# Optimization experiments

Hardware: AMD Instinct MI355X
Metric: run time of the kernel (lower is better)

Reference implementation:

```python
import jax, jax.numpy as jnp
import numpy as np

B, N, Q, H = 32, 1024, 64, 768


def setup_inputs() -> dict:
    key = jax.random.key(0)
    k1, k2, k3, k4 = jax.random.split(key, 4)
    return {
        "nodes_compress": jax.random.normal(k1, (B, N, H), dtype=jnp.float32),
        "query_compress": jax.random.normal(k2, (B, Q, H), dtype=jnp.float32),
        "nodes_hidden": jax.random.normal(k3, (B, N, H), dtype=jnp.float32),
        # nn.Linear(3H, 1, bias=False).weight flattened to (3H,)
        "w": jax.random.normal(k4, (3 * H,), dtype=jnp.float32) * (1.0 / np.sqrt(3 * H)),
    }


def reference(nodes_compress, query_compress, nodes_hidden, w):
    h = nodes_compress.shape[-1]
    w_n, w_q, w_nq = w[:h], w[h:2 * h], w[2 * h:]
    # Decomposed trilinear similarity: identical to Linear([n, q, n*q]) -> scalar
    sim = (
        (nodes_compress @ w_n)[:, :, None]          # (B, N, 1)
        + (query_compress @ w_q)[:, None, :]        # (B, 1, Q)
        + jnp.einsum("bnh,bqh,h->bnq", nodes_compress, query_compress, w_nq)
    )                                                # (B, N, Q)
    # nodes -> query attention
    a = jax.nn.softmax(sim, axis=-1)                 # (B, N, Q)
    nodes2query = jnp.einsum("bnq,bqh->bnh", a, query_compress)
    # query -> nodes attention (max over query, softmax over nodes)
    b = jax.nn.softmax(jnp.max(sim, axis=-1), axis=-1)  # (B, N)
    q2n = jnp.einsum("bn,bnh->bh", b, nodes_compress)[:, None, :]  # (B, 1, H)
    q2n = jnp.broadcast_to(q2n, nodes_compress.shape)               # (B, N, H)
    return jnp.concatenate(
        [nodes_compress, nodes2query, nodes_compress * nodes2query, nodes_compress * q2n],
        axis=-1,
    )  # (B, N, 4H)
```

## Files before the change

### kernel.cpp

```cpp
#include <hip/hip_runtime.h>
#include <hip/hip_bf16.h>

#define BB 32
#define NN 1024
#define QQ 64
#define HH 768

typedef __attribute__((ext_vector_type(8))) short short8;
typedef __attribute__((ext_vector_type(4))) float f32x4;

__device__ __forceinline__ unsigned short f2b(float f) {
  unsigned int u = __float_as_uint(f);
  unsigned int r = u + 0x7fffu + ((u >> 16) & 1u);
  return (unsigned short)(r >> 16);
}

__global__ void k_prep(const float* __restrict__ qc, const float* __restrict__ w,
                       unsigned short* __restrict__ qwB, unsigned short* __restrict__ qcT,
                       float* __restrict__ sq) {
  int bid = blockIdx.x;
  if (bid < 6144) {
    int idx = bid * 256 + threadIdx.x;
    int h = idx % HH;
    qwB[idx] = f2b(qc[idx] * w[2 * HH + h] + w[h]);
    int q2 = idx & 63;
    int h2 = (idx >> 6) % HH;
    int b2 = idx / (HH * QQ);
    qcT[idx] = f2b(qc[(b2 * QQ + q2) * HH + h2]);
  } else {
    int wid = ((bid - 6144) * 256 + threadIdx.x) >> 6;
    int l = threadIdx.x & 63;
    const float* row = qc + (size_t)wid * HH;
    float s = 0.f;
#pragma unroll
    for (int i = 0; i < 12; ++i) s += row[i * 64 + l] * w[HH + i * 64 + l];
#pragma unroll
    for (int m = 1; m < 64; m <<= 1) s += __shfl_xor(s, m);
    if (l == 0) sq[wid] = s;
  }
}

__global__ __launch_bounds__(256) void k_sim(
    const float* __restrict__ nc, const unsigned short* __restrict__ qwB,
    const float* __restrict__ sq, float* __restrict__ partial,
    float* __restrict__ mtse, unsigned short* __restrict__ probs)
{
  __shared__ char smem[32768];
  unsigned short* aLDS = (unsigned short*)smem;
  unsigned short* bLDS = (unsigned short*)(smem + 16384);
  float* rowmF = (float*)(smem + 16384);
  float* wvF   = (float*)(smem + 16384 + 256);

  const int tid = threadIdx.x;
  const int w = tid >> 6, l = tid & 63;
  const int l15 = l & 15, lg = l >> 4;
  const int b = blockIdx.x >> 4, tile = blockIdx.x & 15;
  const int row0 = tile * 64;

  const float* ncB = nc + (size_t)(b * NN + row0) * HH;
  const unsigned short* qwBb = qwB + (size_t)b * QQ * HH;

  f32x4 acc[4] = {};
  for (int kc = 0; kc < 6; ++kc) {
#pragma unroll
    for (int i = 0; i < 4; ++i) {
      int unit = i * 256 + tid;
      int r = unit >> 4, uu = unit & 15;
      const float* src = ncB + r * HH + kc * 128 + uu * 8;
      float4 f0 = *(const float4*)src;
      float4 f1 = *(const float4*)(src + 4);
      short8 v;
      v[0] = (short)f2b(f0.x); v[1] = (short)f2b(f0.y);
      v[2] = (short)f2b(f0.z); v[3] = (short)f2b(f0.w);
      v[4] = (short)f2b(f1.x); v[5] = (short)f2b(f1.y);
      v[6] = (short)f2b(f1.z); v[7] = (short)f2b(f1.w);
      int off = r * 256 + ((uu * 16) ^ ((r & 7) << 4));
      *(short8*)((char*)aLDS + off) = v;
      short8 bv = *(const short8*)(qwBb + r * HH + kc * 128 + uu * 8);
      *(short8*)((char*)bLDS + off) = bv;
    }
    __syncthreads();
#pragma unroll
    for (int ks = 0; ks < 4; ++ks) {
      int kbyte = ks * 64 + lg * 16;
      int arow = w * 16 + l15;
      short8 af = *(short8*)((char*)aLDS + arow * 256 + (kbyte ^ ((l & 7) << 4)));
#pragma unroll
      for (int nt = 0; nt < 4; ++nt) {
        int brow = nt * 16 + l15;
        short8 bf = *(short8*)((char*)bLDS + brow * 256 + (kbyte ^ ((l & 7) << 4)));
        acc[nt] = __builtin_amdgcn_mfma_f32_16x16x32_bf16(af, bf, acc[nt], 0, 0, 0);
      }
      __asm__ volatile("" ::: "memory");
    }
    __syncthreads();
  }

  unsigned short* pT = probs + (size_t)(b * 16 + tile) * (QQ * QQ);
  float sqv[4];
#pragma unroll
  for (int nt = 0; nt < 4; ++nt) sqv[nt] = sq[b * QQ + nt * 16 + l15];
#pragma unroll
  for (int j = 0; j < 4; ++j) {
    float mm = -1e30f;
#pragma unroll
    for (int nt = 0; nt < 4; ++nt) { acc[nt][j] += sqv[nt]; mm = fmaxf(mm, acc[nt][j]); }
    mm = fmaxf(mm, __shfl_xor(mm, 1));
    mm = fmaxf(mm, __shfl_xor(mm, 2));
    mm = fmaxf(mm, __shfl_xor(mm, 4));
    mm = fmaxf(mm, __shfl_xor(mm, 8));
    float ss = 0.f;
#pragma unroll
    for (int nt = 0; nt < 4; ++nt) { float p = __expf(acc[nt][j] - mm); acc[nt][j] = p; ss += p; }
    ss += __shfl_xor(ss, 1); ss += __shfl_xor(ss, 2);
    ss += __shfl_xor(ss, 4); ss += __shfl_xor(ss, 8);
    float inv = 1.0f / ss;
    int r = w * 16 + lg * 4 + j;
#pragma unroll
    for (int nt = 0; nt < 4; ++nt)
      pT[r * 64 + nt * 16 + l15] = f2b(acc[nt][j] * inv);
    if (l15 == 0) rowmF[r] = mm;
  }
  __syncthreads();

  float m_t = -1e30f;
#pragma unroll
  for (int i = 0; i < 16; ++i) {
    f32x4 v = ((f32x4*)rowmF)[i];
    m_t = fmaxf(m_t, fmaxf(fmaxf(v[0], v[1]), fmaxf(v[2], v[3])));
  }
  if (tid < 64) wvF[tid] = __expf(rowmF[tid] - m_t);
  __syncthreads();
  {
    float sv = wvF[l];
#pragma unroll
    for (int m = 1; m < 64; m <<= 1) sv += __shfl_xor(sv, m);
    if (tid == 0) {
      mtse[(b * 16 + tile) * 2] = m_t;
      mtse[(b * 16 + tile) * 2 + 1] = sv;
    }
  }
  {
    float p0 = 0.f, p1 = 0.f, p2 = 0.f;
    for (int n = 0; n < 64; ++n) {
      float wv = wvF[n];
      const float* pr = ncB + n * HH + tid;
      p0 += wv * pr[0]; p1 += wv * pr[256]; p2 += wv * pr[512];
    }
    float* pp = partial + (size_t)(b * 16 + tile) * HH + tid;
    pp[0] = p0; pp[256] = p1; pp[512] = p2;
  }
}

__global__ void k_comb(const float* __restrict__ partial, const float* __restrict__ mtse,
                       float* __restrict__ q2n) {
  int b = blockIdx.x, t = threadIdx.x;
  float mt[16], se[16];
  float M = -1e30f;
#pragma unroll
  for (int i = 0; i < 16; ++i) {
    mt[i] = mtse[(b * 16 + i) * 2];
    se[i] = mtse[(b * 16 + i) * 2 + 1];
    M = fmaxf(M, mt[i]);
  }
  float denom = 0.f;
#pragma unroll
  for (int i = 0; i < 16; ++i) { mt[i] = __expf(mt[i] - M); denom += mt[i] * se[i]; }
  float inv = 1.0f / denom;
  float a0 = 0.f, a1 = 0.f, a2 = 0.f;
#pragma unroll
  for (int i = 0; i < 16; ++i) {
    const float* pp = partial + (size_t)(b * 16 + i) * HH + t;
    float c = mt[i] * inv;
    a0 += c * pp[0]; a1 += c * pp[256]; a2 += c * pp[512];
  }
  q2n[b * HH + t] = a0;
  q2n[b * HH + t + 256] = a1;
  q2n[b * HH + t + 512] = a2;
}

__global__ __launch_bounds__(256) void k_out(
    const float* __restrict__ nc, const unsigned short* __restrict__ qcT,
    const unsigned short* __restrict__ probs, const float* __restrict__ q2n,
    float* __restrict__ out)
{
  __shared__ char smem[16384];

  const int tid = threadIdx.x;
  const int w = tid >> 6, l = tid & 63;
  const int l15 = l & 15, lg = l >> 4;
  const int b = blockIdx.x >> 5;
  const int tile = (blockIdx.x >> 1) & 15;
  const int hh = blockIdx.x & 1;
  const int row0 = tile * 64;

  const unsigned short* pT = probs + (size_t)(b * 16 + tile) * (QQ * QQ);
  short8 a2[2];
  a2[0] = *(const short8*)((const char*)pT + (w * 16 + l15) * 128 + 0 * 64 + lg * 16);
  a2[1] = *(const short8*)((const char*)pT + (w * 16 + l15) * 128 + 1 * 64 + lg * 16);

  const unsigned short* qcTb = qcT + (size_t)b * HH * QQ;
  const int n = w * 16 + l15;
  const float* ncrow = nc + (size_t)(b * NN + row0 + n) * HH;
  float* orow = out + (size_t)(b * NN + row0 + n) * 3072;
  const float* q2nb = q2n + b * HH;

  for (int hc = hh * 3; hc < hh * 3 + 3; ++hc) {
#pragma unroll
    for (int i = 0; i < 4; ++i) {
      int unit = i * 256 + tid;
      int r = unit >> 3, uu = unit & 7;
      short8 v = *(const short8*)(qcTb + (size_t)(hc * 128 + r) * 64 + uu * 8);
      int off = r * 128 + ((uu * 16) ^ ((r & 7) << 4));
      *(short8*)(smem + off) = v;
    }
    __syncthreads();
#pragma unroll
    for (int hg = 0; hg < 8; ++hg) {
      f32x4 c2 = {};
#pragma unroll
      for (int ks2 = 0; ks2 < 2; ++ks2) {
        int hrow = hg * 16 + l15;
        int kbyte = ks2 * 64 + lg * 16;
        short8 hf = *(short8*)(smem + hrow * 128 + (kbyte ^ ((l & 7) << 4)));
        c2 = __builtin_amdgcn_mfma_f32_16x16x32_bf16(hf, a2[ks2], c2, 0, 0, 0);
      }
      int hbase = hc * 128 + hg * 16 + lg * 4;
      f32x4 ncv = *(const f32x4*)(ncrow + hbase);
      f32x4 qv  = *(const f32x4*)(q2nb + hbase);
      __builtin_nontemporal_store(ncv,       (f32x4*)(orow + hbase));
      __builtin_nontemporal_store(c2,        (f32x4*)(orow + HH + hbase));
      __builtin_nontemporal_store(ncv * c2,  (f32x4*)(orow + 2 * HH + hbase));
      __builtin_nontemporal_store(ncv * qv,  (f32x4*)(orow + 2304 + hbase));
    }
    __syncthreads();
  }
}

extern "C" void kernel_launch(void* const* d_in, const int* in_sizes, int n_in,
                              void* d_out, int out_size, void* d_ws, size_t ws_size,
                              hipStream_t stream) {
  (void)in_sizes; (void)n_in; (void)out_size; (void)ws_size;
  const float* nc = (const float*)d_in[0];
  const float* qc = (const float*)d_in[1];
  const float* w  = (const float*)d_in[3];
  float* out = (float*)d_out;
  char* ws = (char*)d_ws;
  unsigned short* qwB = (unsigned short*)(ws);
  unsigned short* qcT = (unsigned short*)(ws + 3145728);
  float* sqv     = (float*)(ws + 6291456);
  float* partial = (float*)(ws + 6299648);
  float* mtse    = (float*)(ws + 7872512);
  float* q2n     = (float*)(ws + 7876608);
  unsigned short* probs = (unsigned short*)(ws + 7975424);

  k_prep<<<6656, 256, 0, stream>>>(qc, w, qwB, qcT, sqv);
  k_sim<<<512, 256, 0, stream>>>(nc, qwB, sqv, partial, mtse, probs);
  k_comb<<<32, 256, 0, stream>>>(partial, mtse, q2n);
  k_out<<<1024, 256, 0, stream>>>(nc, qcT, probs, q2n, out);
}
```

Before: 188.8 us.

## Pre-swizzle operands, pipeline sim loads via direct-to-LDS, fuse combine into output kernel

k_prep now writes qwB and qcT already in the swizzled LDS tile layout, using vectorized per-thread work, so later kernels can copy them with global_load_lds. k_sim double-buffers the B tiles through direct-to-LDS loads and register-prefetches the A rows, converting them straight to MFMA fragments instead of staging A in LDS. It synchronises with manual waitcnt and barriers. The k_comb kernel is removed; each k_out block computes its 128-wide q2n slice from partial/mtse, which repeats that combine work across blocks. k_out grid changes to one block per h-chunk, and stores become regular rather than nontemporal.

```diff
diff --git a/kernel.cpp b/kernel.cpp
--- a/kernel.cpp
+++ b/kernel.cpp
@@ -9,6 +9,10 @@
 typedef __attribute__((ext_vector_type(8))) short short8;
 typedef __attribute__((ext_vector_type(4))) float f32x4;
 
+#define GLOAD_LDS16(gp, lp) \
+  __builtin_amdgcn_global_load_lds((const __attribute__((address_space(1))) unsigned int*)(gp), \
+                                   (__attribute__((address_space(3))) unsigned int*)(lp), 16, 0, 0)
+
 __device__ __forceinline__ unsigned short f2b(float f) {
   unsigned int u = __float_as_uint(f);
   unsigned int r = u + 0x7fffu + ((u >> 16) & 1u);
@@ -18,18 +22,38 @@
 __global__ void k_prep(const float* __restrict__ qc, const float* __restrict__ w,
                        unsigned short* __restrict__ qwB, unsigned short* __restrict__ qcT,
                        float* __restrict__ sq) {
-  int bid = blockIdx.x;
-  if (bid < 6144) {
-    int idx = bid * 256 + threadIdx.x;
-    int h = idx % HH;
-    qwB[idx] = f2b(qc[idx] * w[2 * HH + h] + w[h]);
-    int q2 = idx & 63;
-    int h2 = (idx >> 6) % HH;
-    int b2 = idx / (HH * QQ);
-    qcT[idx] = f2b(qc[(b2 * QQ + q2) * HH + h2]);
+  const int bid = blockIdx.x, tid = threadIdx.x;
+  if (bid < 768) {
+    int gid = bid * 256 + tid;
+    int b = gid / 6144, rem = gid % 6144;
+    int q = rem / 96, kk = rem % 96;
+    int kc = kk >> 4, uu = kk & 15;
+    const float* src = qc + ((size_t)(b * 64 + q) * HH + kk * 8);
+    float4 g0 = *(const float4*)src, g1 = *(const float4*)(src + 4);
+    int h = kk * 8;
+    float4 n0 = *(const float4*)(w + h), n1 = *(const float4*)(w + h + 4);
+    float4 m0 = *(const float4*)(w + 2 * HH + h), m1 = *(const float4*)(w + 2 * HH + h + 4);
+    short8 v;
+    v[0] = (short)f2b(g0.x * m0.x + n0.x); v[1] = (short)f2b(g0.y * m0.y + n0.y);
+    v[2] = (short)f2b(g0.z * m0.z + n0.z); v[3] = (short)f2b(g0.w * m0.w + n0.w);
+    v[4] = (short)f2b(g1.x * m1.x + n1.x); v[5] = (short)f2b(g1.y * m1.y + n1.y);
+    v[6] = (short)f2b(g1.z * m1.z + n1.z); v[7] = (short)f2b(g1.w * m1.w + n1.w);
+    size_t du = (size_t)(b * 6 + kc) * 1024 + q * 16 + (uu ^ (q & 7));
+    *(short8*)((char*)qwB + du * 16) = v;
+  } else if (bid < 1536) {
+    int gid = (bid - 768) * 256 + tid;
+    int b = gid / 6144, p = gid % 6144;
+    int hc = p >> 10, pr = p & 1023, r = pr >> 3, x = pr & 7;
+    int xu = x ^ (r & 7);
+    int h = hc * 128 + r;
+    const float* col = qc + ((size_t)(b * 64 + xu * 8) * HH + h);
+    short8 v;
+#pragma unroll
+    for (int j = 0; j < 8; ++j) v[j] = (short)f2b(col[(size_t)j * HH]);
+    *(short8*)((char*)qcT + (size_t)gid * 16) = v;
   } else {
-    int wid = ((bid - 6144) * 256 + threadIdx.x) >> 6;
-    int l = threadIdx.x & 63;
+    int wid = ((bid - 1536) * 256 + tid) >> 6;
+    int l = tid & 63;
     const float* row = qc + (size_t)wid * HH;
     float s = 0.f;
 #pragma unroll
@@ -45,55 +69,75 @@
     const float* __restrict__ sq, float* __restrict__ partial,
     float* __restrict__ mtse, unsigned short* __restrict__ probs)
 {
-  __shared__ char smem[32768];
-  unsigned short* aLDS = (unsigned short*)smem;
-  unsigned short* bLDS = (unsigned short*)(smem + 16384);
-  float* rowmF = (float*)(smem + 16384);
-  float* wvF   = (float*)(smem + 16384 + 256);
+  __shared__ __align__(16) char bbuf[2][16384];
+  __shared__ float rowmF[64];
+  __shared__ float wvF[64];
 
   const int tid = threadIdx.x;
-  const int w = tid >> 6, l = tid & 63;
+  const int wv_ = tid >> 6, l = tid & 63;
   const int l15 = l & 15, lg = l >> 4;
   const int b = blockIdx.x >> 4, tile = blockIdx.x & 15;
   const int row0 = tile * 64;
 
   const float* ncB = nc + (size_t)(b * NN + row0) * HH;
-  const unsigned short* qwBb = qwB + (size_t)b * QQ * HH;
+  const char* qwb = (const char*)qwB + (size_t)b * 98304;
+  const float* aBase = ncB + (wv_ * 16 + l15) * HH + lg * 8;
+
+  {
+    const char* gsrc = qwb + wv_ * 4096 + l * 16;
+#pragma unroll
+    for (int i = 0; i < 4; ++i)
+      GLOAD_LDS16(gsrc + i * 1024, &bbuf[0][wv_ * 4096 + i * 1024]);
+  }
+  float4 fr[2][8];
+#pragma unroll
+  for (int ks = 0; ks < 4; ++ks) {
+    fr[0][ks * 2]     = *(const float4*)(aBase + ks * 32);
+    fr[0][ks * 2 + 1] = *(const float4*)(aBase + ks * 32 + 4);
+  }
 
   f32x4 acc[4] = {};
+#pragma unroll
   for (int kc = 0; kc < 6; ++kc) {
-#pragma unroll
-    for (int i = 0; i < 4; ++i) {
-      int unit = i * 256 + tid;
-      int r = unit >> 4, uu = unit & 15;
-      const float* src = ncB + r * HH + kc * 128 + uu * 8;
-      float4 f0 = *(const float4*)src;
-      float4 f1 = *(const float4*)(src + 4);
+    short8 af[4];
+#pragma unroll
+    for (int ks = 0; ks < 4; ++ks) {
+      float4 f0 = fr[kc & 1][ks * 2], f1 = fr[kc & 1][ks * 2 + 1];
       short8 v;
       v[0] = (short)f2b(f0.x); v[1] = (short)f2b(f0.y);
       v[2] = (short)f2b(f0.z); v[3] = (short)f2b(f0.w);
       v[4] = (short)f2b(f1.x); v[5] = (short)f2b(f1.y);
       v[6] = (short)f2b(f1.z); v[7] = (short)f2b(f1.w);
-      int off = r * 256 + ((uu * 16) ^ ((r & 7) << 4));
-      *(short8*)((char*)aLDS + off) = v;
-      short8 bv = *(const short8*)(qwBb + r * HH + kc * 128 + uu * 8);
-      *(short8*)((char*)bLDS + off) = bv;
-    }
-    __syncthreads();
+      af[ks] = v;
+    }
+    if (kc < 5) {
+#pragma unroll
+      for (int ks = 0; ks < 4; ++ks) {
+        fr[(kc + 1) & 1][ks * 2]     = *(const float4*)(aBase + (kc + 1) * 128 + ks * 32);
+        fr[(kc + 1) & 1][ks * 2 + 1] = *(const float4*)(aBase + (kc + 1) * 128 + ks * 32 + 4);
+      }
+      const char* gsrc = qwb + (kc + 1) * 16384 + wv_ * 4096 + l * 16;
+#pragma unroll
+      for (int i = 0; i < 4; ++i)
+        GLOAD_LDS16(gsrc + i * 1024, &bbuf[(kc + 1) & 1][wv_ * 4096 + i * 1024]);
+      asm volatile("s_waitcnt vmcnt(12)" ::: "memory");
+    } else {
+      asm volatile("s_waitcnt vmcnt(0)" ::: "memory");
+    }
+    __builtin_amdgcn_s_barrier();
+    __builtin_amdgcn_sched_barrier(0);
 #pragma unroll
     for (int ks = 0; ks < 4; ++ks) {
       int kbyte = ks * 64 + lg * 16;
-      int arow = w * 16 + l15;
-      short8 af = *(short8*)((char*)aLDS + arow * 256 + (kbyte ^ ((l & 7) << 4)));
 #pragma unroll
       for (int nt = 0; nt < 4; ++nt) {
         int brow = nt * 16 + l15;
-        short8 bf = *(short8*)((char*)bLDS + brow * 256 + (kbyte ^ ((l & 7) << 4)));
-        acc[nt] = __builtin_amdgcn_mfma_f32_16x16x32_bf16(af, bf, acc[nt], 0, 0, 0);
+        short8 bf = *(short8*)(&bbuf[kc & 1][0] + brow * 256 + (kbyte ^ ((l & 7) << 4)));
+        acc[nt] = __builtin_amdgcn_mfma_f32_16x16x32_bf16(af[ks], bf, acc[nt], 0, 0, 0);
       }
-      __asm__ volatile("" ::: "memory");
-    }
-    __syncthreads();
+    }
+    __builtin_amdgcn_sched_barrier(0);
+    __builtin_amdgcn_s_barrier();
   }
 
   unsigned short* pT = probs + (size_t)(b * 16 + tile) * (QQ * QQ);
@@ -115,7 +159,7 @@
     ss += __shfl_xor(ss, 1); ss += __shfl_xor(ss, 2);
     ss += __shfl_xor(ss, 4); ss += __shfl_xor(ss, 8);
     float inv = 1.0f / ss;
-    int r = w * 16 + lg * 4 + j;
+    int r = wv_ * 16 + lg * 4 + j;
 #pragma unroll
     for (int nt = 0; nt < 4; ++nt)
       pT[r * 64 + nt * 16 + l15] = f2b(acc[nt][j] * inv);
@@ -143,97 +187,87 @@
   {
     float p0 = 0.f, p1 = 0.f, p2 = 0.f;
     for (int n = 0; n < 64; ++n) {
-      float wv = wvF[n];
+      float wvv = wvF[n];
       const float* pr = ncB + n * HH + tid;
-      p0 += wv * pr[0]; p1 += wv * pr[256]; p2 += wv * pr[512];
+      p0 += wvv * pr[0]; p1 += wvv * pr[256]; p2 += wvv * pr[512];
     }
     float* pp = partial + (size_t)(b * 16 + tile) * HH + tid;
     pp[0] = p0; pp[256] = p1; pp[512] = p2;
   }
 }
 
-__global__ void k_comb(const float* __restrict__ partial, const float* __restrict__ mtse,
-                       float* __restrict__ q2n) {
-  int b = blockIdx.x, t = threadIdx.x;
-  float mt[16], se[16];
-  float M = -1e30f;
-#pragma unroll
-  for (int i = 0; i < 16; ++i) {
-    mt[i] = mtse[(b * 16 + i) * 2];
-    se[i] = mtse[(b * 16 + i) * 2 + 1];
-    M = fmaxf(M, mt[i]);
-  }
-  float denom = 0.f;
-#pragma unroll
-  for (int i = 0; i < 16; ++i) { mt[i] = __expf(mt[i] - M); denom += mt[i] * se[i]; }
-  float inv = 1.0f / denom;
-  float a0 = 0.f, a1 = 0.f, a2 = 0.f;
-#pragma unroll
-  for (int i = 0; i < 16; ++i) {
-    const float* pp = partial + (size_t)(b * 16 + i) * HH + t;
-    float c = mt[i] * inv;
-    a0 += c * pp[0]; a1 += c * pp[256]; a2 += c * pp[512];
-  }
-  q2n[b * HH + t] = a0;
-  q2n[b * HH + t + 256] = a1;
-  q2n[b * HH + t + 512] = a2;
-}
-
 __global__ __launch_bounds__(256) void k_out(
     const float* __restrict__ nc, const unsigned short* __restrict__ qcT,
-    const unsigned short* __restrict__ probs, const float* __restrict__ q2n,
-    float* __restrict__ out)
+    const unsigned short* __restrict__ probs, const float* __restrict__ partial,
+    const float* __restrict__ mtse, float* __restrict__ out)
 {
-  __shared__ char smem[16384];
+  __shared__ __align__(16) char smem[16384];
+  __shared__ float q2nL[128];
 
   const int tid = threadIdx.x;
-  const int w = tid >> 6, l = tid & 63;
+  const int wv_ = tid >> 6, l = tid & 63;
   const int l15 = l & 15, lg = l >> 4;
-  const int b = blockIdx.x >> 5;
-  const int tile = (blockIdx.x >> 1) & 15;
-  const int hh = blockIdx.x & 1;
+  const int bid = blockIdx.x;
+  const int hc = bid % 6;
+  const int bt = bid / 6;
+  const int b = bt >> 4, tile = bt & 15;
   const int row0 = tile * 64;
 
-  const unsigned short* pT = probs + (size_t)(b * 16 + tile) * (QQ * QQ);
-  short8 a2[2];
-  a2[0] = *(const short8*)((const char*)pT + (w * 16 + l15) * 128 + 0 * 64 + lg * 16);
-  a2[1] = *(const short8*)((const char*)pT + (w * 16 + l15) * 128 + 1 * 64 + lg * 16);
-
-  const unsigned short* qcTb = qcT + (size_t)b * HH * QQ;
-  const int n = w * 16 + l15;
+  {
+    const char* src = (const char*)qcT + ((size_t)(b * 6 + hc) << 14) + wv_ * 4096 + l * 16;
+#pragma unroll
+    for (int i = 0; i < 4; ++i)
+      GLOAD_LDS16(src + i * 1024, &smem[wv_ * 4096 + i * 1024]);
+  }
+
+  if (tid < 128) {
+    float M = -1e30f, mt[16], se[16];
+#pragma unroll
+    for (int i = 0; i < 16; ++i) {
+      mt[i] = mtse[(b * 16 + i) * 2];
+      se[i] = mtse[(b * 16 + i) * 2 + 1];
+      M = fmaxf(M, mt[i]);
+    }
+    float denom = 0.f;
+#pragma unroll
+    for (int i = 0; i < 16; ++i) { mt[i] = __expf(mt[i] - M); denom += mt[i] * se[i]; }
+    float inv = 1.0f / denom;
+    float a = 0.f;
+#pragma unroll
+    for (int i = 0; i < 16; ++i)
+      a += mt[i] * partial[(size_t)(b * 16 + i) * HH + hc * 128 + tid];
+    q2nL[tid] = a * inv;
+  }
+
+  const unsigned short* pT = probs + (size_t)bt * (QQ * QQ);
+  short8 a2_0 = *(const short8*)((const char*)pT + (wv_ * 16 + l15) * 128 + lg * 16);
+  short8 a2_1 = *(const short8*)((const char*)pT + (wv_ * 16 + l15) * 128 + 64 + lg * 16);
+
+  asm volatile("s_waitcnt vmcnt(0)" ::: "memory");
+  __syncthreads();
+
+  const int n = wv_ * 16 + l15;
   const float* ncrow = nc + (size_t)(b * NN + row0 + n) * HH;
   float* orow = out + (size_t)(b * NN + row0 + n) * 3072;
-  const float* q2nb = q2n + b * HH;
-
-  for (int hc = hh * 3; hc < hh * 3 + 3; ++hc) {
-#pragma unroll
-    for (int i = 0; i < 4; ++i) {
-      int unit = i * 256 + tid;
-      int r = unit >> 3, uu = unit & 7;
-      short8 v = *(const short8*)(qcTb + (size_t)(hc * 128 + r) * 64 + uu * 8);
-      int off = r * 128 + ((uu * 16) ^ ((r & 7) << 4));
-      *(short8*)(smem + off) = v;
-    }
-    __syncthreads();
-#pragma unroll
-    for (int hg = 0; hg < 8; ++hg) {
-      f32x4 c2 = {};
-#pragma unroll
-      for (int ks2 = 0; ks2 < 2; ++ks2) {
-        int hrow = hg * 16 + l15;
-        int kbyte = ks2 * 64 + lg * 16;
-        short8 hf = *(short8*)(smem + hrow * 128 + (kbyte ^ ((l & 7) << 4)));
-        c2 = __builtin_amdgcn_mfma_f32_16x16x32_bf16(hf, a2[ks2], c2, 0, 0, 0);
-      }
-      int hbase = hc * 128 + hg * 16 + lg * 4;
-      f32x4 ncv = *(const f32x4*)(ncrow + hbase);
-      f32x4 qv  = *(const f32x4*)(q2nb + hbase);
-      __builtin_nontemporal_store(ncv,       (f32x4*)(orow + hbase));
-      __builtin_nontemporal_store(c2,        (f32x4*)(orow + HH + hbase));
-      __builtin_nontemporal_store(ncv * c2,  (f32x4*)(orow + 2 * HH + hbase));
-      __builtin_nontemporal_store(ncv * qv,  (f32x4*)(orow + 2304 + hbase));
-    }
-    __syncthreads();
+
+#pragma unroll
+  for (int hg = 0; hg < 8; ++hg) {
+    f32x4 c2 = {};
+#pragma unroll
+    for (int ks2 = 0; ks2 < 2; ++ks2) {
+      int hrow = hg * 16 + l15;
+      int kbyte = ks2 * 64 + lg * 16;
+      short8 hf = *(short8*)(&smem[0] + hrow * 128 + (kbyte ^ ((l & 7) << 4)));
+      c2 = __builtin_amdgcn_mfma_f32_16x16x32_bf16(hf, ks2 ? a2_1 : a2_0, c2, 0, 0, 0);
+    }
+    int hl = hg * 16 + lg * 4;
+    int hbase = hc * 128 + hl;
+    f32x4 ncv = *(const f32x4*)(ncrow + hbase);
+    f32x4 qv  = *(const f32x4*)(&q2nL[hl]);
+    *(f32x4*)(orow + hbase)          = ncv;
+    *(f32x4*)(orow + HH + hbase)     = c2;
+    *(f32x4*)(orow + 2 * HH + hbase) = ncv * c2;
+    *(f32x4*)(orow + 2304 + hbase)   = ncv * qv;
   }
 }
 
@@ -251,11 +285,9 @@
   float* sqv     = (float*)(ws + 6291456);
   float* partial = (float*)(ws + 6299648);
   float* mtse    = (float*)(ws + 7872512);
-  float* q2n     = (float*)(ws + 7876608);
-  unsigned short* probs = (unsigned short*)(ws + 7975424);
-
-  k_prep<<<6656, 256, 0, stream>>>(qc, w, qwB, qcT, sqv);
+  unsigned short* probs = (unsigned short*)(ws + 7876608);
+
+  k_prep<<<2048, 256, 0, stream>>>(qc, w, qwB, qcT, sqv);
   k_sim<<<512, 256, 0, stream>>>(nc, qwB, sqv, partial, mtse, probs);
-  k_comb<<<32, 256, 0, stream>>>(partial, mtse, q2n);
-  k_out<<<1024, 256, 0, stream>>>(nc, qcT, probs, q2n, out);
-}
+  k_out<<<3072, 256, 0, stream>>>(nc, qcT, probs, partial, mtse, out);
+}
```

Result: faster. 170.1 us (-9.9%).
